# Performance work log

Measured on AMD Instinct MI355X. Metric: run time of the kernel, lower is better.

## Reference

```python
import jax, jax.numpy as jnp
import numpy as np

NUM_EXPERTS = 8
TOP_K = 2
N_EMBD = 1024
BLOCK_SIZE = 128
# d_ffn = round_up(4*n_embd // top_k, block_size)
D_FFN = ((4 * N_EMBD // TOP_K + BLOCK_SIZE - 1) // BLOCK_SIZE) * BLOCK_SIZE  # 2048
TOTAL_WIDTH = NUM_EXPERTS * D_FFN  # 16384


def setup_inputs() -> dict:
    key = jax.random.key(0)
    k1, k2, k3, k4 = jax.random.split(key, 4)
    x = jax.random.normal(k1, (4, 2048, N_EMBD), dtype=jnp.float32)
    # router: nn.Linear(n_embd, num_experts, bias=False) -> weight [E, n_embd]
    w_router = jax.random.normal(k2, (NUM_EXPERTS, N_EMBD), dtype=jnp.float32) * 0.02
    w1 = jax.random.normal(k3, (N_EMBD, TOTAL_WIDTH), dtype=jnp.float32) * 0.02
    w2 = jax.random.normal(k4, (TOTAL_WIDTH, N_EMBD), dtype=jnp.float32) * 0.02
    return {"x": x, "w_router": w_router, "w1": w1, "w2": w2}


def reference(x, w_router, w1, w2):
    B, S, N = x.shape
    T = B * S
    x_flat = x.reshape(T, N)

    # Router
    router_logits = x_flat @ w_router.T                       # [T, E]
    router_probs = jax.nn.softmax(router_logits.astype(jnp.float32), axis=-1)
    expert_weights, selected_experts = jax.lax.top_k(router_probs, TOP_K)  # [T, K]
    # norm_topk_prob=True
    expert_weights = expert_weights / expert_weights.sum(axis=-1, keepdims=True)
    expert_weights = expert_weights.astype(x.dtype)

    # Expert computation. The original does a sort/gather + block-sparse grouped
    # GEMM; math-equivalently, each token's output is
    #   sum_k w_k * gelu(x @ W1_e) @ W2_e  for e = selected_experts[:, k].
    # Loop over the small fixed expert set, masking per-token combine weights.
    out = jnp.zeros((T, N), dtype=x.dtype)
    for e in range(NUM_EXPERTS):
        off = e * D_FFN
        # combine weight for expert e per token (0 if not routed there)
        w_e = jnp.where(selected_experts == e, expert_weights, 0.0).sum(axis=-1)  # [T]
        h = jax.nn.gelu(x_flat @ w1[:, off:off + D_FFN], approximate=False)       # [T, D_FFN]
        out = out + w_e[:, None] * (h @ w2[off:off + D_FFN, :])

    output = out.reshape(B, S, N)

    # Aux losses
    router_z_loss = jnp.mean(jax.nn.logsumexp(router_logits, axis=-1) ** 2)
    p_i = router_probs.mean(axis=0).astype(x.dtype)            # [E]
    flat_sel = selected_experts.reshape(-1)
    f_i = jnp.zeros((NUM_EXPERTS,), dtype=x.dtype).at[flat_sel].add(1.0 / flat_sel.shape[0])
    load_balance_loss = NUM_EXPERTS * (f_i @ p_i)

    return output, router_z_loss, load_balance_loss, f_i
```

## Files before the change

kernel.cpp:

```cpp
#include <hip/hip_runtime.h>
#include <hip/hip_bf16.h>
#include <math.h>

#define T_TOK 8192
#define NE 1024
#define N_EXP 8
#define DFFN 2048
#define TW 16384
#define P_TOT 16384

#define BMT 128
#define BNT 128
#define BK9 32

typedef __attribute__((ext_vector_type(8))) short bf16x8;
typedef __attribute__((ext_vector_type(4))) float f32x4;

#define GLOAD_LDS16(g, l) __builtin_amdgcn_global_load_lds( \
    (const __attribute__((address_space(1))) void*)(g), \
    (__attribute__((address_space(3))) void*)(l), 16, 0, 0)

static __device__ __forceinline__ unsigned short f2bf(float f) {
    __hip_bfloat16 b = __float2bfloat16(f);
    return *(unsigned short*)&b;
}

static __device__ __forceinline__ float gelu_fast(float v) {
    float u2 = v * (1.5957691216f + 0.0713548162f * v * v);
    return v / (1.f + __expf(-u2));
}

__global__ __launch_bounds__(256) void router_kernel(
    const float* __restrict__ x, const float* __restrict__ wr,
    int* __restrict__ sel_idx, float* __restrict__ sel_wt,
    float* __restrict__ z_part, float* __restrict__ p_part)
{
    __shared__ float wrs[N_EXP * NE];
    __shared__ float zred[32];
    __shared__ float pred[32][8];
    int tid = threadIdx.x;
    for (int i = tid; i < N_EXP * NE / 4; i += 256)
        ((float4*)wrs)[i] = ((const float4*)wr)[i];
    __syncthreads();

    int slot = tid >> 3, oct = tid & 7;
    int t = blockIdx.x * 32 + slot;
    float lg[N_EXP];
#pragma unroll
    for (int e = 0; e < N_EXP; e++) lg[e] = 0.f;

    const float4* x4 = (const float4*)(x + (size_t)t * NE) + oct * 32;
    for (int n4 = 0; n4 < 32; n4++) {
        float4 xv = x4[n4];
#pragma unroll
        for (int e = 0; e < N_EXP; e++) {
            const float* w = &wrs[e * NE + oct * 128 + n4 * 4];
            lg[e] += xv.x * w[0] + xv.y * w[1] + xv.z * w[2] + xv.w * w[3];
        }
    }
#pragma unroll
    for (int d = 1; d < 8; d <<= 1)
#pragma unroll
        for (int e = 0; e < N_EXP; e++) lg[e] += __shfl_xor(lg[e], d);

    float m = lg[0];
#pragma unroll
    for (int e = 1; e < N_EXP; e++) m = fmaxf(m, lg[e]);
    float p[N_EXP], s = 0.f;
#pragma unroll
    for (int e = 0; e < N_EXP; e++) { p[e] = expf(lg[e] - m); s += p[e]; }
    float inv = 1.f / s;
#pragma unroll
    for (int e = 0; e < N_EXP; e++) p[e] *= inv;
    float lse = m + logf(s);

    int e0 = 0;
#pragma unroll
    for (int e = 1; e < N_EXP; e++) if (p[e] > p[e0]) e0 = e;
    int e1 = (e0 == 0) ? 1 : 0;
#pragma unroll
    for (int e = 0; e < N_EXP; e++) if (e != e0 && p[e] > p[e1]) e1 = e;

    if (oct == 0) {
        float wn = 1.f / (p[e0] + p[e1]);
        sel_idx[t * 2 + 0] = e0;
        sel_idx[t * 2 + 1] = e1;
        sel_wt[t * 2 + 0] = p[e0] * wn;
        sel_wt[t * 2 + 1] = p[e1] * wn;
        zred[slot] = lse * lse;
#pragma unroll
        for (int e = 0; e < N_EXP; e++) pred[slot][e] = p[e];
    }
    __syncthreads();
    if (tid == 0) {
        float zs = 0.f;
        for (int i = 0; i < 32; i++) zs += zred[i];
        z_part[blockIdx.x] = zs;
        for (int e = 0; e < N_EXP; e++) {
            float ps = 0.f;
            for (int i = 0; i < 32; i++) ps += pred[i][e];
            p_part[blockIdx.x * N_EXP + e] = ps;
        }
    }
}

__global__ __launch_bounds__(256) void finalize_router(
    const int* __restrict__ sel_idx,
    const float* __restrict__ z_part, const float* __restrict__ p_part,
    int* __restrict__ cnt, int* __restrict__ off, int* __restrict__ cursor,
    int* __restrict__ tile_tab, int* __restrict__ tile_n,
    float* __restrict__ out)
{
    __shared__ int redc[256];
    __shared__ int cnts[N_EXP];
    int tid = threadIdx.x;
    int c[N_EXP];
#pragma unroll
    for (int e = 0; e < N_EXP; e++) c[e] = 0;
    for (int i = tid; i < P_TOT; i += 256) c[sel_idx[i]]++;
#pragma unroll
    for (int e = 0; e < N_EXP; e++) {
        redc[tid] = c[e];
        __syncthreads();
        for (int st = 128; st > 0; st >>= 1) {
            if (tid < st) redc[tid] += redc[tid + st];
            __syncthreads();
        }
        if (tid == 0) cnts[e] = redc[0];
        __syncthreads();
    }
    if (tid == 0) {
        int o = 0;
        int nt = 0;
        for (int e = 0; e < N_EXP; e++) {
            cnt[e] = cnts[e];
            off[e] = o;
            o += cnts[e];
            cursor[e] = 0;
            for (int rb = 0; rb < cnts[e]; rb += BMT)
                tile_tab[nt++] = (e << 20) | rb;
        }
        off[N_EXP] = o;
        tile_n[0] = nt;
        float zs = 0.f;
        for (int b = 0; b < 256; b++) zs += z_part[b];
        float lb = 0.f;
        float* tail = out + (size_t)T_TOK * NE;
        for (int e = 0; e < N_EXP; e++) {
            float ps = 0.f;
            for (int b = 0; b < 256; b++) ps += p_part[b * N_EXP + e];
            float fi = (float)cnts[e] / (float)P_TOT;
            float pi = ps / (float)T_TOK;
            lb += fi * pi;
            tail[2 + e] = fi;
        }
        tail[0] = zs / (float)T_TOK;
        tail[1] = 8.f * lb;
    }
}

__global__ __launch_bounds__(256) void scatter_kernel(
    const int* __restrict__ sel_idx, const int* __restrict__ off,
    int* __restrict__ cursor, int* __restrict__ token_list)
{
    int i = blockIdx.x * 256 + threadIdx.x;
    if (i < P_TOT) {
        int e = sel_idx[i];
        int pos = atomicAdd(&cursor[e], 1);
        token_list[off[e] + pos] = i;
    }
}

__global__ __launch_bounds__(256) void cvt_x_kernel(
    const float* __restrict__ x, unsigned short* __restrict__ xb)
{
    int i = blockIdx.x * 256 + threadIdx.x;
    float4 v = ((const float4*)x)[i];
    ushort4 o;
    o.x = f2bf(v.x); o.y = f2bf(v.y); o.z = f2bf(v.z); o.w = f2bf(v.w);
    ((ushort4*)xb)[i] = o;
}

__global__ __launch_bounds__(256) void transpose_bf16_kernel(
    const float* __restrict__ src, unsigned short* __restrict__ dst,
    int R, int C)
{
    __shared__ float tile[64][65];
    int rb = blockIdx.y * 64, cb = blockIdx.x * 64;
    int tid = threadIdx.x;
#pragma unroll
    for (int p = 0; p < 4; p++) {
        int idx = p * 256 + tid;
        int r = idx >> 4, c4 = (idx & 15) << 2;
        float4 v = *(const float4*)&src[(size_t)(rb + r) * C + cb + c4];
        tile[r][c4 + 0] = v.x; tile[r][c4 + 1] = v.y;
        tile[r][c4 + 2] = v.z; tile[r][c4 + 3] = v.w;
    }
    __syncthreads();
#pragma unroll
    for (int p = 0; p < 4; p++) {
        int idx = p * 256 + tid;
        int c = idx >> 4, r4 = (idx & 15) << 2;
        ushort4 o;
        o.x = f2bf(tile[r4 + 0][c]); o.y = f2bf(tile[r4 + 1][c]);
        o.z = f2bf(tile[r4 + 2][c]); o.w = f2bf(tile[r4 + 3][c]);
        *(ushort4*)&dst[(size_t)(cb + c) * R + rb + r4] = o;
    }
}

#define STG(buf, kb) do {                                                 \
    GLOAD_LDS16(asrc0 + (kb), &As[buf][wid * 1024]);                      \
    GLOAD_LDS16(asrc1 + (kb), &As[buf][wid * 1024 + 512]);                \
    GLOAD_LDS16(bsrc0 + (kb), &Bs[buf][wid * 1024]);                      \
    GLOAD_LDS16(bsrc1 + (kb), &Bs[buf][wid * 1024 + 512]);                \
} while (0)

#define GEMM_LOOP(NKT)                                                    \
    STG(0, 0);                                                            \
    for (int t = 0; t < (NKT); t++) {                                     \
        int cur = t & 1;                                                  \
        if (t + 1 < (NKT)) {                                              \
            STG(cur ^ 1, (t + 1) * BK9);                                  \
            asm volatile("s_waitcnt vmcnt(4)" ::: "memory");              \
        } else {                                                          \
            asm volatile("s_waitcnt vmcnt(0)" ::: "memory");              \
        }                                                                 \
        __builtin_amdgcn_s_barrier();                                     \
        __builtin_amdgcn_sched_barrier(0);                                \
        bf16x8 af[4], bfr[4];                                             \
        _Pragma("unroll")                                                 \
        for (int m = 0; m < 4; m++)                                       \
            af[m] = *(const bf16x8*)&As[cur][(wm * 64 + m * 16 + rr) * BK9 + kqa * 8]; \
        _Pragma("unroll")                                                 \
        for (int n = 0; n < 4; n++)                                       \
            bfr[n] = *(const bf16x8*)&Bs[cur][(wn * 64 + n * 16 + rr) * BK9 + kqa * 8]; \
        _Pragma("unroll")                                                 \
        for (int m = 0; m < 4; m++)                                       \
            _Pragma("unroll")                                             \
            for (int n = 0; n < 4; n++)                                   \
                acc[m][n] = __builtin_amdgcn_mfma_f32_16x16x32_bf16(      \
                    af[m], bfr[n], acc[m][n], 0, 0, 0);                   \
        __builtin_amdgcn_sched_barrier(0);                                \
        __builtin_amdgcn_s_barrier();                                     \
    }

__global__ __launch_bounds__(256, 4) void gemm1_mfma(
    const __hip_bfloat16* __restrict__ xb, const __hip_bfloat16* __restrict__ w1t,
    const int* __restrict__ token_list, const float* __restrict__ sel_wt,
    const int* __restrict__ cnt, const int* __restrict__ off,
    const int* __restrict__ tile_tab, const int* __restrict__ tile_n,
    __hip_bfloat16* __restrict__ h)
{
    __shared__ __align__(16) __hip_bfloat16 As[2][BMT * BK9];
    __shared__ __align__(16) __hip_bfloat16 Bs[2][BNT * BK9];

    int flat = blockIdx.x;
    if (flat >= tile_n[0]) return;
    int tab = tile_tab[flat];
    int e = tab >> 20, rowbase = tab & 0xFFFFF;
    int off_e = off[e];
    int rows_e = cnt[e] - rowbase;
    int colbase = blockIdx.y * BNT;

    int tid = threadIdx.x;
    int wid = tid >> 6, lane = tid & 63;
    int wm = wid >> 1, wn = wid & 1;
    int rr = lane & 15, kq = lane >> 4;
    int kqa = kq ^ ((rr >> 1) & 3);
    int ksw = (lane & 3) ^ ((lane >> 3) & 3);

    int r0 = wid * 32 + (lane >> 2);
    int r1 = r0 + 16;
    int ent0 = token_list[off_e + rowbase + ((r0 < rows_e) ? r0 : 0)];
    int ent1 = token_list[off_e + rowbase + ((r1 < rows_e) ? r1 : 0)];
    const __hip_bfloat16* asrc0 = xb + (size_t)(ent0 >> 1) * NE + ksw * 8;
    const __hip_bfloat16* asrc1 = xb + (size_t)(ent1 >> 1) * NE + ksw * 8;
    const __hip_bfloat16* bsrc0 = w1t + (size_t)(e * DFFN + colbase + r0) * NE + ksw * 8;
    const __hip_bfloat16* bsrc1 = bsrc0 + (size_t)16 * NE;

    f32x4 acc[4][4] = {};
    GEMM_LOOP(NE / BK9)

    int colg = colbase + wn * 64;
#pragma unroll
    for (int m = 0; m < 4; m++) {
#pragma unroll
        for (int j = 0; j < 4; j++) {
            int r = wm * 64 + m * 16 + kq * 4 + j;
            if (r < rows_e) {
                size_t p = (size_t)off_e + rowbase + r;
                float wgt = sel_wt[token_list[p]];
#pragma unroll
                for (int n = 0; n < 4; n++) {
                    float g = gelu_fast(acc[m][n][j]);
                    h[p * DFFN + colg + n * 16 + rr] = __float2bfloat16(wgt * g);
                }
            }
        }
    }
}

__global__ __launch_bounds__(256, 4) void gemm2_mfma(
    const __hip_bfloat16* __restrict__ h, const __hip_bfloat16* __restrict__ w2t,
    const int* __restrict__ token_list,
    const int* __restrict__ cnt, const int* __restrict__ off,
    const int* __restrict__ tile_tab, const int* __restrict__ tile_n,
    float* __restrict__ out)
{
    __shared__ __align__(16) __hip_bfloat16 As[2][BMT * BK9];
    __shared__ __align__(16) __hip_bfloat16 Bs[2][BNT * BK9];

    int flat = blockIdx.x;
    if (flat >= tile_n[0]) return;
    int tab = tile_tab[flat];
    int e = tab >> 20, rowbase = tab & 0xFFFFF;
    int off_e = off[e];
    int rows_e = cnt[e] - rowbase;
    int colbase = blockIdx.y * BNT;

    int tid = threadIdx.x;
    int wid = tid >> 6, lane = tid & 63;
    int wm = wid >> 1, wn = wid & 1;
    int rr = lane & 15, kq = lane >> 4;
    int kqa = kq ^ ((rr >> 1) & 3);
    int ksw = (lane & 3) ^ ((lane >> 3) & 3);

    int r0 = wid * 32 + (lane >> 2);
    int r1 = r0 + 16;
    int pr0 = off_e + rowbase + ((r0 < rows_e) ? r0 : 0);
    int pr1 = off_e + rowbase + ((r1 < rows_e) ? r1 : 0);
    const __hip_bfloat16* asrc0 = h + (size_t)pr0 * DFFN + ksw * 8;
    const __hip_bfloat16* asrc1 = h + (size_t)pr1 * DFFN + ksw * 8;
    const __hip_bfloat16* bsrc0 = w2t + (size_t)(colbase + r0) * TW + e * DFFN + ksw * 8;
    const __hip_bfloat16* bsrc1 = bsrc0 + (size_t)16 * TW;

    f32x4 acc[4][4] = {};
    GEMM_LOOP(DFFN / BK9)

    int colg = colbase + wn * 64;
#pragma unroll
    for (int m = 0; m < 4; m++) {
#pragma unroll
        for (int j = 0; j < 4; j++) {
            int r = wm * 64 + m * 16 + kq * 4 + j;
            if (r < rows_e) {
                size_t p = (size_t)off_e + rowbase + r;
                int tok = token_list[p] >> 1;
#pragma unroll
                for (int n = 0; n < 4; n++)
                    atomicAdd(&out[(size_t)tok * NE + colg + n * 16 + rr],
                              acc[m][n][j]);
            }
        }
    }
}

extern "C" void kernel_launch(void* const* d_in, const int* in_sizes, int n_in,
                              void* d_out, int out_size, void* d_ws, size_t ws_size,
                              hipStream_t stream)
{
    const float* x  = (const float*)d_in[0];
    const float* wr = (const float*)d_in[1];
    const float* w1 = (const float*)d_in[2];
    const float* w2 = (const float*)d_in[3];
    float* out = (float*)d_out;

    char* ws = (char*)d_ws;
    size_t o = 0;
    __hip_bfloat16* h   = (__hip_bfloat16*)(ws + o); o += (size_t)P_TOT * DFFN * 2;
    __hip_bfloat16* xb  = (__hip_bfloat16*)(ws + o); o += (size_t)T_TOK * NE * 2;
    __hip_bfloat16* w1t = (__hip_bfloat16*)(ws + o); o += (size_t)NE * TW * 2;
    __hip_bfloat16* w2t = (__hip_bfloat16*)(ws + o); o += (size_t)TW * NE * 2;
    int*   sel_idx    = (int*)(ws + o);   o += P_TOT * 4;
    float* sel_wt     = (float*)(ws + o); o += P_TOT * 4;
    int*   token_list = (int*)(ws + o);   o += P_TOT * 4;
    int*   cnt        = (int*)(ws + o);   o += 64;
    int*   off        = (int*)(ws + o);   o += 64;
    int*   cursor     = (int*)(ws + o);   o += 64;
    int*   tile_tab   = (int*)(ws + o);   o += 256 * 4;
    int*   tile_n     = (int*)(ws + o);   o += 64;
    float* z_part     = (float*)(ws + o); o += 256 * 4;
    float* p_part     = (float*)(ws + o); o += 256 * N_EXP * 4;

    hipMemsetAsync(d_out, 0, (size_t)out_size * sizeof(float), stream);

    cvt_x_kernel<<<T_TOK * NE / 4 / 256, 256, 0, stream>>>(x, (unsigned short*)xb);
    transpose_bf16_kernel<<<dim3(TW / 64, NE / 64), 256, 0, stream>>>(
        w1, (unsigned short*)w1t, NE, TW);
    transpose_bf16_kernel<<<dim3(NE / 64, TW / 64), 256, 0, stream>>>(
        w2, (unsigned short*)w2t, TW, NE);

    router_kernel<<<256, 256, 0, stream>>>(x, wr, sel_idx, sel_wt, z_part, p_part);
    finalize_router<<<1, 256, 0, stream>>>(sel_idx, z_part, p_part, cnt, off, cursor,
                                           tile_tab, tile_n, out);
    scatter_kernel<<<64, 256, 0, stream>>>(sel_idx, off, cursor, token_list);

    gemm1_mfma<<<dim3(136, DFFN / BNT), 256, 0, stream>>>(
        xb, w1t, token_list, sel_wt, cnt, off, tile_tab, tile_n, h);
    gemm2_mfma<<<dim3(136, NE / BNT), 256, 0, stream>>>(
        h, w2t, token_list, cnt, off, tile_tab, tile_n, out);
}
```

Measured before the change: 455.5 us.

## Fuse bf16 conversion into router, remap GEMM grids per XCD, raise MFMA priority

Converts x to bf16 inside the router kernel while it already reads x, removing a separate conversion pass and one launch. GEMM grids are flattened to 1D, and the block index is decoded so consecutive blocks, which are likely spread across the 8 XCDs, handle different column tiles of the same row tile, aiming to improve L2 reuse of the A rows. s_setprio is raised around the MFMA block so compute-bound waves are favored over loads. The router now writes extra data, which could slow that kernel a little.

```diff
diff --git a/kernel.cpp b/kernel.cpp
--- a/kernel.cpp
+++ b/kernel.cpp
@@ -33,7 +33,8 @@
 __global__ __launch_bounds__(256) void router_kernel(
     const float* __restrict__ x, const float* __restrict__ wr,
     int* __restrict__ sel_idx, float* __restrict__ sel_wt,
-    float* __restrict__ z_part, float* __restrict__ p_part)
+    float* __restrict__ z_part, float* __restrict__ p_part,
+    unsigned short* __restrict__ xb)
 {
     __shared__ float wrs[N_EXP * NE];
     __shared__ float zred[32];
@@ -52,6 +53,9 @@
     const float4* x4 = (const float4*)(x + (size_t)t * NE) + oct * 32;
     for (int n4 = 0; n4 < 32; n4++) {
         float4 xv = x4[n4];
+        ushort4 o;
+        o.x = f2bf(xv.x); o.y = f2bf(xv.y); o.z = f2bf(xv.z); o.w = f2bf(xv.w);
+        *(ushort4*)&xb[(size_t)t * NE + oct * 128 + n4 * 4] = o;
 #pragma unroll
         for (int e = 0; e < N_EXP; e++) {
             const float* w = &wrs[e * NE + oct * 128 + n4 * 4];
@@ -169,16 +173,6 @@
         int pos = atomicAdd(&cursor[e], 1);
         token_list[off[e] + pos] = i;
     }
-}
-
-__global__ __launch_bounds__(256) void cvt_x_kernel(
-    const float* __restrict__ x, unsigned short* __restrict__ xb)
-{
-    int i = blockIdx.x * 256 + threadIdx.x;
-    float4 v = ((const float4*)x)[i];
-    ushort4 o;
-    o.x = f2bf(v.x); o.y = f2bf(v.y); o.z = f2bf(v.z); o.w = f2bf(v.w);
-    ((ushort4*)xb)[i] = o;
 }
 
 __global__ __launch_bounds__(256) void transpose_bf16_kernel(
@@ -234,12 +228,14 @@
         _Pragma("unroll")                                                 \
         for (int n = 0; n < 4; n++)                                       \
             bfr[n] = *(const bf16x8*)&Bs[cur][(wn * 64 + n * 16 + rr) * BK9 + kqa * 8]; \
+        __builtin_amdgcn_s_setprio(1);                                    \
         _Pragma("unroll")                                                 \
         for (int m = 0; m < 4; m++)                                       \
             _Pragma("unroll")                                             \
             for (int n = 0; n < 4; n++)                                   \
                 acc[m][n] = __builtin_amdgcn_mfma_f32_16x16x32_bf16(      \
                     af[m], bfr[n], acc[m][n], 0, 0, 0);                   \
+        __builtin_amdgcn_s_setprio(0);                                    \
         __builtin_amdgcn_sched_barrier(0);                                \
         __builtin_amdgcn_s_barrier();                                     \
     }
@@ -254,13 +250,15 @@
     __shared__ __align__(16) __hip_bfloat16 As[2][BMT * BK9];
     __shared__ __align__(16) __hip_bfloat16 Bs[2][BNT * BK9];
 
-    int flat = blockIdx.x;
-    if (flat >= tile_n[0]) return;
-    int tab = tile_tab[flat];
+    int b = blockIdx.x;
+    int slot = b & 7, idx = b >> 3;
+    int rowt = idx >> 1;
+    if (rowt >= tile_n[0]) return;
+    int colbase = (slot * 2 + (idx & 1)) * BNT;
+    int tab = tile_tab[rowt];
     int e = tab >> 20, rowbase = tab & 0xFFFFF;
     int off_e = off[e];
     int rows_e = cnt[e] - rowbase;
-    int colbase = blockIdx.y * BNT;
 
     int tid = threadIdx.x;
     int wid = tid >> 6, lane = tid & 63;
@@ -310,13 +308,14 @@
     __shared__ __align__(16) __hip_bfloat16 As[2][BMT * BK9];
     __shared__ __align__(16) __hip_bfloat16 Bs[2][BNT * BK9];
 
-    int flat = blockIdx.x;
-    if (flat >= tile_n[0]) return;
-    int tab = tile_tab[flat];
+    int b = blockIdx.x;
+    int slot = b & 7, rowt = b >> 3;
+    if (rowt >= tile_n[0]) return;
+    int colbase = slot * BNT;
+    int tab = tile_tab[rowt];
     int e = tab >> 20, rowbase = tab & 0xFFFFF;
     int off_e = off[e];
     int rows_e = cnt[e] - rowbase;
-    int colbase = blockIdx.y * BNT;
 
     int tid = threadIdx.x;
     int wid = tid >> 6, lane = tid & 63;
@@ -384,19 +383,18 @@
 
     hipMemsetAsync(d_out, 0, (size_t)out_size * sizeof(float), stream);
 
-    cvt_x_kernel<<<T_TOK * NE / 4 / 256, 256, 0, stream>>>(x, (unsigned short*)xb);
+    router_kernel<<<256, 256, 0, stream>>>(x, wr, sel_idx, sel_wt, z_part, p_part,
+                                           (unsigned short*)xb);
     transpose_bf16_kernel<<<dim3(TW / 64, NE / 64), 256, 0, stream>>>(
         w1, (unsigned short*)w1t, NE, TW);
     transpose_bf16_kernel<<<dim3(NE / 64, TW / 64), 256, 0, stream>>>(
         w2, (unsigned short*)w2t, TW, NE);
-
-    router_kernel<<<256, 256, 0, stream>>>(x, wr, sel_idx, sel_wt, z_part, p_part);
     finalize_router<<<1, 256, 0, stream>>>(sel_idx, z_part, p_part, cnt, off, cursor,
                                            tile_tab, tile_n, out);
     scatter_kernel<<<64, 256, 0, stream>>>(sel_idx, off, cursor, token_list);
 
-    gemm1_mfma<<<dim3(136, DFFN / BNT), 256, 0, stream>>>(
+    gemm1_mfma<<<2176, 256, 0, stream>>>(
         xb, w1t, token_list, sel_wt, cnt, off, tile_tab, tile_n, h);
-    gemm2_mfma<<<dim3(136, NE / BNT), 256, 0, stream>>>(
+    gemm2_mfma<<<1088, 256, 0, stream>>>(
         h, w2t, token_list, cnt, off, tile_tab, tile_n, out);
 }
```

Result: faster. 441.2 us (-3.1%).
